# Optimization experiments

Measured on AMD Instinct MI355X. Metric: run time of the kernel, lower is better.

Reference implementation:

```python
import jax, jax.numpy as jnp
import numpy as np


def _idxct_last(x):
    """IDCT-like transform along the last axis (DREAMPlace idxct):
        y_u = sum_{k=0}^{N-1} x_k * cos(pi * k * (u + 0.5) / N)
    computed via the Makhoul FFT trick: phase-twiddle + length-N IFFT + even/odd reorder.
    """
    N = x.shape[-1]
    k = jnp.arange(N)
    # twiddle: exp(i*pi*k/(2N))  (this is what dct_cpp/dct_cuda precompute as expk)
    phase = jnp.exp(1j * jnp.pi * k.astype(jnp.float32) / (2.0 * N)).astype(jnp.complex64)
    z = x.astype(jnp.complex64) * phase
    # f_n = sum_k z_k exp(+i 2pi k n / N)  == N * ifft(z)
    v = jnp.real(jnp.fft.ifft(z, axis=-1)) * N
    half = (N + 1) // 2
    # de-interleave: y[2i] = v[i], y[2i+1] = v[N-1-i]
    y = jnp.zeros_like(x)
    y = y.at[..., 0::2].set(v[..., :half].astype(x.dtype))
    y = y.at[..., 1::2].set(jnp.flip(v[..., half:], axis=-1).astype(x.dtype))
    return y


def idcct2_math(x):
    """2D inverse discrete cosine-cosine transform (separable):
        y_{u,v} = sum_{p,q} x_{p,q} cos(pi p (u+0.5)/M) cos(pi q (v+0.5)/N)
    equivalent to idxct(idxct(x)^T)^T.
    """
    y = _idxct_last(x)                      # transform along last dim (N)
    y = _idxct_last(jnp.swapaxes(y, -1, -2))  # transform along first dim (M)
    return jnp.swapaxes(y, -1, -2)


def setup_inputs() -> dict:
    key = jax.random.key(0)
    M, N = 4096, 4096
    x = jax.random.normal(key, (M, N), dtype=jnp.float32)
    return {"x": x}


def reference(x):
    return idcct2_math(x)
```

## Files before the change

### kernel.cpp

```cpp
#include <hip/hip_runtime.h>
#include <hip/hip_bf16.h>

typedef unsigned short u16;
typedef u16 us4 __attribute__((ext_vector_type(4)));
typedef u16 us8 __attribute__((ext_vector_type(8)));
typedef __bf16 bf16x8 __attribute__((ext_vector_type(8)));
typedef float f32x4 __attribute__((ext_vector_type(4)));

#define NDIM 4096
#define HDIM 2048

__device__ __forceinline__ u16 bfbits(float f) {
    __hip_bfloat16 h = __float2bfloat16(f);
    return __builtin_bit_cast(u16, h);
}
__device__ __forceinline__ float bf2f(u16 b) {
    return __builtin_bit_cast(float, ((unsigned)b) << 16);
}

__device__ __forceinline__ void gload_lds16(const u16* g, u16* l) {
    __builtin_amdgcn_global_load_lds((__attribute__((address_space(1))) void*)g,
                                     (__attribute__((address_space(3))) void*)l,
                                     16, 0, 0);
}

__global__ __launch_bounds__(256) void k_gencos2(u16* __restrict__ Ce, u16* __restrict__ Co) {
    int idx = blockIdx.x * 256 + threadIdx.x;
    int u = idx >> 8;
    int k0 = (idx & 255) * 8;
    unsigned step = (unsigned)(2 * u + 1);
    us8 e, o;
#pragma unroll
    for (int i = 0; i < 8; ++i) {
        unsigned kk = (unsigned)(k0 + i);
        unsigned te = (2u * kk * step) & 16383u;
        unsigned to = ((2u * kk + 1u) * step) & 16383u;
        e[i] = bfbits(cosf((float)te * 3.8349519697141029e-4f));
        o[i] = bfbits(cosf((float)to * 3.8349519697141029e-4f));
    }
    *(us8*)&Ce[(size_t)idx * 8] = e;
    *(us8*)&Co[(size_t)idx * 8] = o;
}

__global__ __launch_bounds__(256) void k_transpose_split(const float* __restrict__ X,
                                                         u16* __restrict__ Xe,
                                                         u16* __restrict__ Xo) {
    __shared__ float tile[64][65];
    int b  = blockIdx.x;
    int bx = (b & 63) * 64;
    int by = (b >> 6) * 64;
    int t  = threadIdx.x;
    int lr = t >> 4, lc = (t & 15) * 4;
#pragma unroll
    for (int r = 0; r < 64; r += 16) {
        float4 v = *(const float4*)&X[(size_t)(by + lr + r) * NDIM + bx + lc];
        tile[lr + r][lc + 0] = v.x;
        tile[lr + r][lc + 1] = v.y;
        tile[lr + r][lc + 2] = v.z;
        tile[lr + r][lc + 3] = v.w;
    }
    __syncthreads();
    int jl = t >> 2;
    int s8 = (t & 3) * 8;
    us8 e, o;
#pragma unroll
    for (int i = 0; i < 8; ++i) {
        e[i] = bfbits(tile[2 * (s8 + i)][jl]);
        o[i] = bfbits(tile[2 * (s8 + i) + 1][jl]);
    }
    size_t base = (size_t)(bx + jl) * HDIM + (by >> 1) + s8;
    *(us8*)&Xe[base] = e;
    *(us8*)&Xo[base] = o;
}

__global__ __launch_bounds__(256) void k_bfly1(const u16* __restrict__ S,
                                               const u16* __restrict__ D,
                                               u16* __restrict__ We,
                                               u16* __restrict__ Wo) {
    int idx = blockIdx.x * 256 + threadIdx.x;
    int u  = idx >> 9;
    int j0 = (idx & 511) * 8;
    us8 s8 = *(const us8*)&S[(size_t)u * NDIM + j0];
    us8 d8 = *(const us8*)&D[(size_t)u * NDIM + j0];
    us4 et, ot, eb, ob;
#pragma unroll
    for (int i = 0; i < 4; ++i) {
        float se = bf2f(s8[2 * i]),     de = bf2f(d8[2 * i]);
        float so = bf2f(s8[2 * i + 1]), dd = bf2f(d8[2 * i + 1]);
        et[i] = bfbits(se + de);  eb[i] = bfbits(se - de);
        ot[i] = bfbits(so + dd);  ob[i] = bfbits(so - dd);
    }
    size_t ct = (size_t)u * HDIM + (j0 >> 1);
    size_t cb = (size_t)(NDIM - 1 - u) * HDIM + (j0 >> 1);
    *(us4*)&We[ct] = et;  *(us4*)&Wo[ct] = ot;
    *(us4*)&We[cb] = eb;  *(us4*)&Wo[cb] = ob;
}

__global__ __launch_bounds__(256) void k_bfly2(const u16* __restrict__ S2,
                                               const u16* __restrict__ D2,
                                               float* __restrict__ Y) {
    int idx = blockIdx.x * 256 + threadIdx.x;
    int i  = idx >> 8;
    int v0 = (idx & 255) * 8;
    us8 s8 = *(const us8*)&S2[(size_t)i * HDIM + v0];
    us8 d8 = *(const us8*)&D2[(size_t)i * HDIM + v0];
    float sum[8], dif[8];
#pragma unroll
    for (int t = 0; t < 8; ++t) {
        float s = bf2f(s8[t]), d = bf2f(d8[t]);
        sum[t] = s + d;  dif[t] = s - d;
    }
    f32x4 a0, a1, r0, r1;
#pragma unroll
    for (int w = 0; w < 4; ++w) {
        a0[w] = sum[w];  a1[w] = sum[w + 4];
        r0[w] = dif[7 - w];  r1[w] = dif[3 - w];
    }
    float* row = Y + (size_t)i * NDIM;
    *(f32x4*)&row[v0]           = a0;
    *(f32x4*)&row[v0 + 4]       = a1;
    *(f32x4*)&row[4088 - v0]    = r0;
    *(f32x4*)&row[4092 - v0]    = r1;
}

#define BAR() do { asm volatile("" ::: "memory"); __builtin_amdgcn_s_barrier(); \
                   asm volatile("" ::: "memory"); } while (0)

template <int NTK, int LOG_NTN>
__global__ __launch_bounds__(512, 2) void gemm256h(const u16* __restrict__ A0,
                                                   const u16* __restrict__ A1,
                                                   const u16* __restrict__ B0,
                                                   const u16* __restrict__ B1,
                                                   u16* __restrict__ out) {
    constexpr int KD  = NTK * 64;
    constexpr int NTN = 1 << LOG_NTN;
    constexpr int LDC = NTN * 256;
    constexpr int MTILES = 128 >> LOG_NTN;

    __shared__ u16 As[2 * 256 * 64];
    __shared__ u16 Bs[2 * 256 * 64];

    const int tid  = threadIdx.x;
    const int wave = tid >> 6;
    const int lane = tid & 63;

    const int bid = blockIdx.x;
    const int swz = (bid & 7) * 32 + (bid >> 3);
    const int half = swz >> 7;
    const int r    = swz & 127;
    const int bm   = (r >> LOG_NTN) * 256;
    const int bn   = (r & (NTN - 1)) * 256;

    const u16* A = half ? A1 : A0;
    const u16* B = half ? B1 : B0;
    u16* Cp = out + (size_t)half * MTILES * 256 * LDC;

    const int wr = wave >> 2;
    const int wc = wave & 3;

    const int srow = lane >> 3;
    const int scol = ((lane & 7) ^ srow) << 3;

    const int fr   = lane & 15;
    const int hi   = lane >> 4;
    const int slot0 = ((hi)     ^ (lane & 7)) << 3;
    const int slot1 = ((hi + 4) ^ (lane & 7)) << 3;
    const int aRow = (wr * 128 + fr) * 64;
    const int bRow = (wc * 64 + fr) * 64;

    f32x4 acc[8][4] = {};
    bf16x8 aR[4][2], b01[2][2], b23[2][2];

#define STAGE(LARR, GP, ORG, H, TK, BOFF)                                       \
    do {                                                                        \
        const int _tk = (TK) & (NTK - 1);                                       \
        _Pragma("unroll")                                                       \
        for (int q = 0; q < 2; ++q) {                                           \
            const u16* _g = (GP) + (size_t)((ORG) + (H) * 128 +                 \
                             (wave * 2 + q) * 8 + srow) * KD + _tk * 64 + scol; \
            gload_lds16(_g, LARR + (BOFF) + (H) * 8192 + (wave * 2 + q) * 512 + lane * 8); \
        }                                                                       \
    } while (0)

#define LOAD_A(MB, BOFF)                                                        \
    _Pragma("unroll")                                                           \
    for (int mm = 0; mm < 4; ++mm) {                                            \
        aR[mm][0] = __builtin_bit_cast(bf16x8, *(const us8*)(As + (BOFF) + aRow + ((MB) + mm) * 1024 + slot0)); \
        aR[mm][1] = __builtin_bit_cast(bf16x8, *(const us8*)(As + (BOFF) + aRow + ((MB) + mm) * 1024 + slot1)); \
    }

#define LOAD_B(DST, NB, BOFF)                                                   \
    _Pragma("unroll")                                                           \
    for (int nn = 0; nn < 2; ++nn) {                                            \
        DST[nn][0] = __builtin_bit_cast(bf16x8, *(const us8*)(Bs + (BOFF) + bRow + ((NB) + nn) * 1024 + slot0)); \
        DST[nn][1] = __builtin_bit_cast(bf16x8, *(const us8*)(Bs + (BOFF) + bRow + ((NB) + nn) * 1024 + slot1)); \
    }

#define MFMA_Q(MB, NB, BREG)                                                    \
    do {                                                                        \
        __builtin_amdgcn_s_setprio(1);                                          \
        _Pragma("unroll")                                                       \
        for (int mm = 0; mm < 4; ++mm)                                          \
            _Pragma("unroll")                                                   \
            for (int nn = 0; nn < 2; ++nn) {                                    \
                acc[(MB)+mm][(NB)+nn] = __builtin_amdgcn_mfma_f32_16x16x32_bf16(aR[mm][0], BREG[nn][0], acc[(MB)+mm][(NB)+nn], 0, 0, 0); \
                acc[(MB)+mm][(NB)+nn] = __builtin_amdgcn_mfma_f32_16x16x32_bf16(aR[mm][1], BREG[nn][1], acc[(MB)+mm][(NB)+nn], 0, 0, 0); \
            }                                                                   \
        __builtin_amdgcn_s_setprio(0);                                          \
    } while (0)

    STAGE(Bs, B, bn, 0, 0, 0);
    STAGE(Bs, B, bn, 1, 0, 0);
    STAGE(As, A, bm, 0, 0, 0);
    STAGE(As, A, bm, 1, 0, 0);
    STAGE(Bs, B, bn, 0, 1, 16384);
    STAGE(Bs, B, bn, 1, 1, 16384);
    asm volatile("s_waitcnt vmcnt(4)" ::: "memory");
    BAR();

    for (int t = 0; t < NTK; t += 2) {
        LOAD_A(0, 0);
        LOAD_B(b01, 0, 0);
        STAGE(As, A, bm, 0, t + 1, 16384);
        BAR();
        MFMA_Q(0, 0, b01);
        BAR();
        LOAD_B(b23, 2, 0);
        STAGE(As, A, bm, 1, t + 1, 16384);
        BAR();
        MFMA_Q(0, 2, b23);
        BAR();
        LOAD_A(4, 0);
        STAGE(Bs, B, bn, 0, t + 2, 0);
        BAR();
        MFMA_Q(4, 2, b23);
        BAR();
        STAGE(Bs, B, bn, 1, t + 2, 0);
        BAR();
        MFMA_Q(4, 0, b01);
        asm volatile("s_waitcnt vmcnt(4)" ::: "memory");
        BAR();
        LOAD_A(0, 16384);
        LOAD_B(b01, 0, 16384);
        STAGE(As, A, bm, 0, t + 2, 0);
        BAR();
        MFMA_Q(0, 0, b01);
        BAR();
        LOAD_B(b23, 2, 16384);
        STAGE(As, A, bm, 1, t + 2, 0);
        BAR();
        MFMA_Q(0, 2, b23);
        BAR();
        LOAD_A(4, 16384);
        STAGE(Bs, B, bn, 0, t + 3, 16384);
        BAR();
        MFMA_Q(4, 2, b23);
        BAR();
        STAGE(Bs, B, bn, 1, t + 3, 16384);
        BAR();
        MFMA_Q(4, 0, b01);
        asm volatile("s_waitcnt vmcnt(4)" ::: "memory");
        BAR();
    }

    asm volatile("s_waitcnt vmcnt(0)" ::: "memory");

    const int orow0 = wr * 128 + hi * 4;
    const int ocol0 = bn + wc * 64 + fr;
#pragma unroll
    for (int m = 0; m < 8; ++m)
#pragma unroll
        for (int n = 0; n < 4; ++n) {
            f32x4 v = acc[m][n];
#pragma unroll
            for (int rr = 0; rr < 4; ++rr) {
                size_t off = (size_t)(bm + orow0 + m * 16 + rr) * LDC + (ocol0 + n * 16);
                Cp[off] = bfbits(v[rr]);
            }
        }
#undef STAGE
#undef LOAD_A
#undef LOAD_B
#undef MFMA_Q
}

extern "C" void kernel_launch(void* const* d_in, const int* in_sizes, int n_in,
                              void* d_out, int out_size, void* d_ws, size_t ws_size,
                              hipStream_t stream) {
    const float* X = (const float*)d_in[0];
    float* Y = (float*)d_out;

    const size_t QM = (size_t)HDIM * HDIM;
    u16* Ce = (u16*)d_ws;
    u16* Co = Ce + QM;
    u16* Xe = Co + QM;
    u16* Xo = Xe + 2 * QM;
    u16* S  = Xo + 2 * QM;
    u16* D  = S + 2 * QM;
    u16* We = Xe;
    u16* Wo = Xo;
    u16* S2 = S;
    u16* D2 = D;

    k_gencos2<<<2048, 256, 0, stream>>>(Ce, Co);
    k_transpose_split<<<4096, 256, 0, stream>>>(X, Xe, Xo);
    gemm256h<32, 4><<<256, 512, 0, stream>>>(Ce, Co, Xe, Xo, S);
    k_bfly1<<<4096, 256, 0, stream>>>(S, D, We, Wo);
    gemm256h<32, 3><<<256, 512, 0, stream>>>(We, Wo, Ce, Co, S2);
    k_bfly2<<<4096, 256, 0, stream>>>(S2, D2, Y);
}
```

Before: 178.4 us.

## Restage GEMM LDS loads by consumption-order halves to prefetch earlier

Measured after the change: 174.3 us. 1.02x faster.

```diff
diff --git a/kernel.cpp b/kernel.cpp
--- a/kernel.cpp
+++ b/kernel.cpp
@@ -117,14 +117,15 @@
         r0[w] = dif[7 - w];  r1[w] = dif[3 - w];
     }
     float* row = Y + (size_t)i * NDIM;
-    *(f32x4*)&row[v0]           = a0;
-    *(f32x4*)&row[v0 + 4]       = a1;
-    *(f32x4*)&row[4088 - v0]    = r0;
-    *(f32x4*)&row[4092 - v0]    = r1;
+    *(f32x4*)&row[v0]        = a0;
+    *(f32x4*)&row[v0 + 4]    = a1;
+    *(f32x4*)&row[4088 - v0] = r0;
+    *(f32x4*)&row[4092 - v0] = r1;
 }
 
 #define BAR() do { asm volatile("" ::: "memory"); __builtin_amdgcn_s_barrier(); \
                    asm volatile("" ::: "memory"); } while (0)
+#define WAITV(N) asm volatile("s_waitcnt vmcnt(" #N ")" ::: "memory")
 
 template <int NTK, int LOG_NTN>
 __global__ __launch_bounds__(512, 2) void gemm256h(const u16* __restrict__ A0,
@@ -168,18 +169,32 @@
     const int aRow = (wr * 128 + fr) * 64;
     const int bRow = (wc * 64 + fr) * 64;
 
+
     f32x4 acc[8][4] = {};
     bf16x8 aR[4][2], b01[2][2], b23[2][2];
 
-#define STAGE(LARR, GP, ORG, H, TK, BOFF)                                       \
-    do {                                                                        \
-        const int _tk = (TK) & (NTK - 1);                                       \
-        _Pragma("unroll")                                                       \
-        for (int q = 0; q < 2; ++q) {                                           \
-            const u16* _g = (GP) + (size_t)((ORG) + (H) * 128 +                 \
-                             (wave * 2 + q) * 8 + srow) * KD + _tk * 64 + scol; \
-            gload_lds16(_g, LARR + (BOFF) + (H) * 8192 + (wave * 2 + q) * 512 + lane * 8); \
-        }                                                                       \
+#define STAGE_A(TK, H, BOFF)                                                     \
+    do {                                                                         \
+        const int _tk = (TK) & (NTK - 1);                                        \
+        _Pragma("unroll")                                                        \
+        for (int q = 0; q < 2; ++q) {                                            \
+            const int seg  = wave * 2 + q;                                       \
+            const int row0 = (H) * 64 + (seg & 7) * 8 + (seg >> 3) * 128;        \
+            const u16* _g = A + (size_t)(bm + row0 + srow) * KD + _tk * 64 + scol; \
+            gload_lds16(_g, As + (BOFF) + row0 * 64 + lane * 8);                 \
+        }                                                                        \
+    } while (0)
+
+#define STAGE_B(TK, H, BOFF)                                                     \
+    do {                                                                         \
+        const int _tk = (TK) & (NTK - 1);                                        \
+        _Pragma("unroll")                                                        \
+        for (int q = 0; q < 2; ++q) {                                            \
+            const int seg  = wave * 2 + q;                                       \
+            const int row0 = (H) * 32 + (seg & 3) * 8 + (seg >> 2) * 64;         \
+            const u16* _g = B + (size_t)(bn + row0 + srow) * KD + _tk * 64 + scol; \
+            gload_lds16(_g, Bs + (BOFF) + row0 * 64 + lane * 8);                 \
+        }                                                                        \
     } while (0)
 
 #define LOAD_A(MB, BOFF)                                                        \
@@ -209,57 +224,58 @@
         __builtin_amdgcn_s_setprio(0);                                          \
     } while (0)
 
-    STAGE(Bs, B, bn, 0, 0, 0);
-    STAGE(Bs, B, bn, 1, 0, 0);
-    STAGE(As, A, bm, 0, 0, 0);
-    STAGE(As, A, bm, 1, 0, 0);
-    STAGE(Bs, B, bn, 0, 1, 16384);
-    STAGE(Bs, B, bn, 1, 1, 16384);
-    asm volatile("s_waitcnt vmcnt(4)" ::: "memory");
+    STAGE_B(0, 0, 0);
+    STAGE_A(0, 0, 0);
+    STAGE_B(0, 1, 0);
+    STAGE_A(0, 1, 0);
+    STAGE_B(1, 0, 16384);
+    STAGE_A(1, 0, 16384);
+    STAGE_B(1, 1, 16384);
+    WAITV(6);
     BAR();
 
     for (int t = 0; t < NTK; t += 2) {
         LOAD_A(0, 0);
         LOAD_B(b01, 0, 0);
-        STAGE(As, A, bm, 0, t + 1, 16384);
+        STAGE_A(t + 1, 1, 16384);
         BAR();
         MFMA_Q(0, 0, b01);
         BAR();
         LOAD_B(b23, 2, 0);
-        STAGE(As, A, bm, 1, t + 1, 16384);
+        STAGE_B(t + 2, 0, 0);
         BAR();
         MFMA_Q(0, 2, b23);
         BAR();
         LOAD_A(4, 0);
-        STAGE(Bs, B, bn, 0, t + 2, 0);
+        STAGE_A(t + 2, 0, 0);
         BAR();
         MFMA_Q(4, 2, b23);
         BAR();
-        STAGE(Bs, B, bn, 1, t + 2, 0);
+        STAGE_B(t + 2, 1, 0);
         BAR();
         MFMA_Q(4, 0, b01);
-        asm volatile("s_waitcnt vmcnt(4)" ::: "memory");
+        WAITV(6);
         BAR();
         LOAD_A(0, 16384);
         LOAD_B(b01, 0, 16384);
-        STAGE(As, A, bm, 0, t + 2, 0);
+        STAGE_A(t + 2, 1, 0);
         BAR();
         MFMA_Q(0, 0, b01);
         BAR();
         LOAD_B(b23, 2, 16384);
-        STAGE(As, A, bm, 1, t + 2, 0);
+        STAGE_B(t + 3, 0, 16384);
         BAR();
         MFMA_Q(0, 2, b23);
         BAR();
         LOAD_A(4, 16384);
-        STAGE(Bs, B, bn, 0, t + 3, 16384);
+        STAGE_A(t + 3, 0, 16384);
         BAR();
         MFMA_Q(4, 2, b23);
         BAR();
-        STAGE(Bs, B, bn, 1, t + 3, 16384);
+        STAGE_B(t + 3, 1, 16384);
         BAR();
         MFMA_Q(4, 0, b01);
-        asm volatile("s_waitcnt vmcnt(4)" ::: "memory");
+        WAITV(6);
         BAR();
     }
 
@@ -278,7 +294,8 @@
                 Cp[off] = bfbits(v[rr]);
             }
         }
-#undef STAGE
+#undef STAGE_A
+#undef STAGE_B
 #undef LOAD_A
 #undef LOAD_B
 #undef MFMA_Q
```
